# Kernel tuning notes

Hardware: AMD Instinct MI355X
Metric: run time of the kernel (lower is better)

Reference implementation:

```python
import jax, jax.numpy as jnp
import numpy as np

N = 50000      # nodes
E = 800000     # edges (avg degree 16)
DIN = 128
H = 128
DOUT = 64


def setup_inputs() -> dict:
    key = jax.random.key(0)
    ks = jax.random.split(key, 8)
    x = jax.random.normal(ks[0], (N, DIN), dtype=jnp.float32)
    edge_index = jax.random.randint(ks[1], (2, E), 0, N, dtype=jnp.int32)
    def glorot(k, fi, fo):
        return jax.random.normal(k, (fi, fo), dtype=jnp.float32) * (1.0 / np.sqrt(fi))
    return {
        "x": x,
        "edge_index": edge_index,
        "W1": glorot(ks[2], DIN, H), "b1": jnp.zeros((H,), jnp.float32),
        "W2": glorot(ks[3], H, H),   "b2": jnp.zeros((H,), jnp.float32),
        "W3": glorot(ks[4], H, DOUT),"b3": jnp.zeros((DOUT,), jnp.float32),
    }


def reference(x, edge_index, W1, b1, W2, b2, W3, b3):
    n = x.shape[0]
    # GCNConv: add self-loops, symmetric degree normalization D^-1/2 (A+I) D^-1/2
    loop = jnp.arange(n, dtype=edge_index.dtype)
    src = jnp.concatenate([edge_index[0], loop])  # [E+N]
    dst = jnp.concatenate([edge_index[1], loop])
    deg = jax.ops.segment_sum(jnp.ones(src.shape, x.dtype), dst, num_segments=n)
    dinv = jnp.where(deg > 0, jax.lax.rsqrt(deg), 0.0)
    norm = dinv[src] * dinv[dst]  # [E+N]

    def conv(h, W, b):
        h = h @ W                                   # [N, out]
        msg = h[src] * norm[:, None]                # gather + scale
        return jax.ops.segment_sum(msg, dst, num_segments=n) + b

    # gelu after every layer except the last (forward breaks before act)
    h = jax.nn.gelu(conv(x, W1, b1), approximate=False)
    h = jax.nn.gelu(conv(h, W2, b2), approximate=False)
    return conv(h, W3, b3)
```

## Files before the change

### kernel.cpp

```cpp
#include <hip/hip_runtime.h>
#include <math.h>

#define NDIN 128
#define NHID 128
#define NDOUT 64

typedef _Float16 half2_t __attribute__((ext_vector_type(2)));
typedef _Float16 half4_t __attribute__((ext_vector_type(4)));
typedef _Float16 half8_t __attribute__((ext_vector_type(8)));
typedef float    float4v __attribute__((ext_vector_type(4)));

__device__ __forceinline__ float gelu_exact(float x) {
    return 0.5f * x * (1.0f + erff(x * 0.70710678118654752f));
}


__device__ void wtrans_tile(const float* __restrict__ W, _Float16* __restrict__ Wt,
                            int K, int N, int bx, int by) {
    __shared__ float tile[32][33];
    int tx = threadIdx.x & 31, ty = threadIdx.x >> 5;
    for (int i = 0; i < 32; i += 8) {
        int k = by * 32 + ty + i, nn = bx * 32 + tx;
        tile[ty + i][tx] = (k < K && nn < N) ? W[(size_t)k * N + nn] : 0.f;
    }
    __syncthreads();
    for (int i = 0; i < 32; i += 8) {
        int nn = bx * 32 + ty + i, k = by * 32 + tx;
        if (nn < N && k < K) Wt[(size_t)nn * K + k] = (_Float16)tile[tx][ty + i];
    }
}

__global__ __launch_bounds__(256) void prep0_kernel(
    const float* __restrict__ W1, _Float16* __restrict__ W1t,
    const float* __restrict__ W2, _Float16* __restrict__ W2t,
    const float* __restrict__ W3, _Float16* __restrict__ W3t,
    int* __restrict__ count, int* __restrict__ done, int n) {
    int b = blockIdx.x;
    if (b < 16) {
        wtrans_tile(W1, W1t, NDIN, NHID, b & 3, b >> 2);
    } else if (b < 32) {
        wtrans_tile(W2, W2t, NHID, NHID, (b - 16) & 3, (b - 16) >> 2);
    } else if (b < 40) {
        wtrans_tile(W3, W3t, NHID, NDOUT, (b - 32) & 1, (b - 32) >> 1);
    } else {
        int z = b - 40;
        int i = z * 256 + threadIdx.x;
        if (i < n) count[i] = 0;
        if (z == 0 && threadIdx.x < 64) done[threadIdx.x] = 0;
    }
}


__global__ void count_kernel(const int* __restrict__ dst, int* __restrict__ count, int E) {
    int e = blockIdx.x * blockDim.x + threadIdx.x;
    if (e < E) atomicAdd(&count[dst[e]], 1);
}


__global__ __launch_bounds__(256) void reduce_scan_kernel(
    const int* __restrict__ count, int* __restrict__ blocksum, int* __restrict__ blockoff,
    int* __restrict__ rowptr, float* __restrict__ dinv, int* __restrict__ done,
    int nb, int n) {
    __shared__ int s[256];
    __shared__ int flag;
    __shared__ int boff_s;
    int t = threadIdx.x;
    int i = blockIdx.x * 256 + t;
    int v = (i < n) ? count[i] : 0;
    s[t] = v;
    __syncthreads();
    for (int off = 128; off > 0; off >>= 1) {
        if (t < off) s[t] += s[t + off];
        __syncthreads();
    }
    if (t == 0) {
        atomicExch(&blocksum[blockIdx.x], s[0]);
        __threadfence();
        int old = atomicAdd(&done[0], 1);
        flag = (old == nb - 1) ? 1 : 0;
    }
    __syncthreads();
    if (flag) {
        __threadfence();
        int pv = (t < nb) ? atomicAdd(&blocksum[t], 0) : 0;
        s[t] = pv;
        __syncthreads();
        for (int off = 1; off < 256; off <<= 1) {
            int u = (t >= off) ? s[t - off] : 0;
            __syncthreads();
            s[t] += u;
            __syncthreads();
        }
        if (t < nb) atomicExch(&blockoff[t], s[t] - pv);
        if (t == 255) rowptr[n] = s[255];
        __threadfence();
        if (t == 0) atomicExch(&done[1], 1);
    } else if (t == 0) {
        while (atomicAdd(&done[1], 0) == 0) __builtin_amdgcn_s_sleep(2);
        __threadfence();
    }
    __syncthreads();
    if (t == 0) boff_s = atomicAdd(&blockoff[blockIdx.x], 0);
    s[t] = v;
    __syncthreads();
    for (int off = 1; off < 256; off <<= 1) {
        int u = (t >= off) ? s[t - off] : 0;
        __syncthreads();
        s[t] += u;
        __syncthreads();
    }
    if (i < n) {
        rowptr[i] = boff_s + s[t] - v;
        dinv[i] = rsqrtf((float)(v + 1));
    }
}


template <int BN>
__device__ __forceinline__ void gemm_phaseB(
    const _Float16 (*lds_a)[136], const _Float16* __restrict__ Bt,
    _Float16* __restrict__ T, int bm, int M) {
    int tid = threadIdx.x;
    int wave = tid >> 6, lane = tid & 63;
    int m = lane & 15, quad = lane >> 4;
    const int NT = BN / 16;
    float4v acc[NT];
#pragma unroll
    for (int nt = 0; nt < NT; nt++) acc[nt] = (float4v){0.f, 0.f, 0.f, 0.f};
    int arow = (wave << 4) + m;
#pragma unroll
    for (int kc = 0; kc < 128; kc += 32) {
        half8_t a = *(const half8_t*)&lds_a[arow][kc + quad * 8];
#pragma unroll
        for (int nt = 0; nt < NT; nt++) {
            half8_t b = *(const half8_t*)&Bt[(size_t)(nt * 16 + m) * 128 + kc + quad * 8];
            acc[nt] = __builtin_amdgcn_mfma_f32_16x16x32_f16(a, b, acc[nt], 0, 0, 0);
        }
    }
#pragma unroll
    for (int nt = 0; nt < NT; nt++) {
#pragma unroll
        for (int r = 0; r < 4; r++) {
            int grow = bm + (wave << 4) + (quad << 2) + r;
            if (grow < M) T[(size_t)grow * BN + nt * 16 + m] = (_Float16)acc[nt][r];
        }
    }
}


__device__ __forceinline__ half2_t agg_node128(
    const half2_t* __restrict__ t2, const int* __restrict__ rowptr,
    const int2* __restrict__ adj, const float* __restrict__ dinv,
    const float* __restrict__ bias, int node, int lane) {
    float wself = dinv[node];
    wself *= wself;
    half2_t v = t2[(size_t)node * 64 + lane];
    float accx = wself * (float)v[0], accy = wself * (float)v[1];
    int beg = rowptr[node], end = rowptr[node + 1];
    for (int e0 = beg; e0 < end; e0 += 64) {
        int rem = end - e0;
        int j = 0; float w = 0.f;
        if (lane < rem) {
            int2 ed = adj[e0 + lane];
            j = ed.x; w = __int_as_float(ed.y);
        }
        int cnt = rem < 64 ? rem : 64;
        for (int c = 0; c < cnt; c += 16) {
#pragma unroll
            for (int i = 0; i < 16; i++) {
                int jj = __builtin_amdgcn_readlane(j, c + i);
                float ww = __int_as_float(
                    __builtin_amdgcn_readlane(__float_as_int(w), c + i));
                half2_t u = t2[(size_t)jj * 64 + lane];
                accx += ww * (float)u[0];
                accy += ww * (float)u[1];
            }
        }
    }
    float2 b = ((const float2*)bias)[lane];
    accx = gelu_exact(accx + b.x);
    accy = gelu_exact(accy + b.y);
    half2_t o; o[0] = (_Float16)accx; o[1] = (_Float16)accy;
    return o;
}


__global__ __launch_bounds__(256) void fill_gemm1_kernel(
    const int* __restrict__ src, const int* __restrict__ dst,
    const float* __restrict__ dinv, const int* __restrict__ rowptr,
    int* __restrict__ count, int2* __restrict__ adj, int E,
    const float* __restrict__ x, const _Float16* __restrict__ W1t,
    _Float16* __restrict__ T, int M, int fillblocks) {
    __shared__ _Float16 lds_a[64][136];
    int b = blockIdx.x;
    if (b < fillblocks) {
        int e = b * 256 + threadIdx.x;
        if (e >= E) return;
        int s = src[e], d = dst[e];
        int slot = atomicSub(&count[d], 1) - 1;
        int p = rowptr[d] + slot;
        adj[p] = make_int2(s, __float_as_int(dinv[s] * dinv[d]));
        return;
    }
    int bm = (b - fillblocks) * 64;
    int tid = threadIdx.x;
#pragma unroll
    for (int j = 0; j < 8; j++) {
        int c = tid + j * 256;
        int r = c >> 5, col = (c & 31) << 2;
        int grow = bm + r;
        float4 v = make_float4(0.f, 0.f, 0.f, 0.f);
        if (grow < M) v = *(const float4*)(x + (size_t)grow * 128 + col);
        half4_t h;
        h[0] = (_Float16)v.x; h[1] = (_Float16)v.y;
        h[2] = (_Float16)v.z; h[3] = (_Float16)v.w;
        *(half4_t*)&lds_a[r][col] = h;
    }
    __syncthreads();
    gemm_phaseB<128>(lds_a, W1t, T, bm, M);
}


template <int BN>
__global__ __launch_bounds__(256, 4) void agg_gemm_kernel(
    const _Float16* __restrict__ t, const int* __restrict__ rowptr,
    const int2* __restrict__ adj, const float* __restrict__ dinv,
    const float* __restrict__ bias, const _Float16* __restrict__ Bt,
    _Float16* __restrict__ T, int M) {
    __shared__ _Float16 lds_a[64][136];
    int tid = threadIdx.x;
    int wave = tid >> 6, lane = tid & 63;
    int bm = blockIdx.x * 64;
    const half2_t* t2 = (const half2_t*)t;
#pragma unroll 1
    for (int p = 0; p < 16; p++) {
        int r = (wave << 4) + p;
        int node = bm + r;
        half2_t o;
        o[0] = (_Float16)0.f; o[1] = (_Float16)0.f;
        if (node < M) o = agg_node128(t2, rowptr, adj, dinv, bias, node, lane);
        *(half2_t*)&lds_a[r][lane << 1] = o;
    }
    __syncthreads();
    gemm_phaseB<BN>(lds_a, Bt, T, bm, M);
}


template <int F, bool DOGELU, bool OUTF16>
__global__ __launch_bounds__(256) void agg_kernel(
    const _Float16* __restrict__ t, const int* __restrict__ rowptr,
    const int2* __restrict__ adj, const float* __restrict__ dinv,
    const float* __restrict__ bias, void* __restrict__ outp, int n) {
    int node = (int)((blockIdx.x * blockDim.x + threadIdx.x) >> 6);
    int lane = threadIdx.x & 63;
    if (node >= n) return;

    float wself = dinv[node];
    wself *= wself;
    int beg = rowptr[node];
    int end = rowptr[node + 1];

    if (F == 128) {
        const half2_t* t2 = (const half2_t*)t;
        half2_t v = t2[(size_t)node * 64 + lane];
        float accx = wself * (float)v[0], accy = wself * (float)v[1];
        for (int e0 = beg; e0 < end; e0 += 64) {
            int rem = end - e0;
            int j = 0; float w = 0.f;
            if (lane < rem) {
                int2 ed = adj[e0 + lane];
                j = ed.x; w = __int_as_float(ed.y);
            }
            int cnt = rem < 64 ? rem : 64;
            for (int c = 0; c < cnt; c += 16) {
#pragma unroll
                for (int i = 0; i < 16; i++) {
                    int jj = __builtin_amdgcn_readlane(j, c + i);
                    float ww = __int_as_float(
                        __builtin_amdgcn_readlane(__float_as_int(w), c + i));
                    half2_t u = t2[(size_t)jj * 64 + lane];
                    accx += ww * (float)u[0];
                    accy += ww * (float)u[1];
                }
            }
        }
        float2 b = ((const float2*)bias)[lane];
        accx += b.x; accy += b.y;
        if (DOGELU) { accx = gelu_exact(accx); accy = gelu_exact(accy); }
        if (OUTF16) {
            half2_t o; o[0] = (_Float16)accx; o[1] = (_Float16)accy;
            ((half2_t*)outp)[(size_t)node * 64 + lane] = o;
        } else {
            float2 o; o.x = accx; o.y = accy;
            ((float2*)outp)[(size_t)node * 64 + lane] = o;
        }
    } else {
        float acc = wself * (float)t[(size_t)node * 64 + lane];
        for (int e0 = beg; e0 < end; e0 += 64) {
            int rem = end - e0;
            int j = 0; float w = 0.f;
            if (lane < rem) {
                int2 ed = adj[e0 + lane];
                j = ed.x; w = __int_as_float(ed.y);
            }
            int cnt = rem < 64 ? rem : 64;
            for (int c = 0; c < cnt; c += 16) {
#pragma unroll
                for (int i = 0; i < 16; i++) {
                    int jj = __builtin_amdgcn_readlane(j, c + i);
                    float ww = __int_as_float(
                        __builtin_amdgcn_readlane(__float_as_int(w), c + i));
                    acc += ww * (float)t[(size_t)jj * 64 + lane];
                }
            }
        }
        acc += bias[lane];
        if (DOGELU) acc = gelu_exact(acc);
        if (OUTF16) ((_Float16*)outp)[(size_t)node * 64 + lane] = (_Float16)acc;
        else        ((float*)outp)[(size_t)node * 64 + lane] = acc;
    }
}


extern "C" void kernel_launch(void* const* d_in, const int* in_sizes, int n_in,
                              void* d_out, int out_size, void* d_ws, size_t ws_size,
                              hipStream_t stream) {
    const float* x  = (const float*)d_in[0];
    const int* edge = (const int*)d_in[1];
    const float* W1 = (const float*)d_in[2];
    const float* b1 = (const float*)d_in[3];
    const float* W2 = (const float*)d_in[4];
    const float* b2 = (const float*)d_in[5];
    const float* W3 = (const float*)d_in[6];
    const float* b3 = (const float*)d_in[7];
    float* out = (float*)d_out;

    const int N = in_sizes[0] / NDIN;
    const int E = in_sizes[1] / 2;
    const int* src = edge;
    const int* dst = edge + E;
    const int NB = (N + 255) / 256;

    char* p = (char*)d_ws;
    auto alloc = [&](size_t bytes) {
        char* q = p;
        p += (bytes + 255) & ~(size_t)255;
        return q;
    };
    int*       count    = (int*)alloc((size_t)N * 4);
    int*       rowptr   = (int*)alloc((size_t)(N + 1) * 4);
    int*       blocksum = (int*)alloc((size_t)NB * 4);
    int*       blockoff = (int*)alloc((size_t)NB * 4);
    int*       done     = (int*)alloc(256);
    float*     dinv     = (float*)alloc((size_t)N * 4);
    int2*      adj      = (int2*)alloc((size_t)E * 8);
    _Float16*  W1t      = (_Float16*)alloc((size_t)NHID * NDIN * 2);
    _Float16*  W2t      = (_Float16*)alloc((size_t)NHID * NHID * 2);
    _Float16*  W3t      = (_Float16*)alloc((size_t)NDOUT * NHID * 2);
    _Float16*  tbuf     = (_Float16*)alloc((size_t)N * NHID * 2);
    _Float16*  hbuf     = (_Float16*)alloc((size_t)N * NHID * 2);

    dim3 blk(256);
    int mtiles = (N + 63) / 64;
    int eblocks = (E + 255) / 256;
    int agg_blocks = (N + 3) / 4;

    prep0_kernel<<<40 + NB, blk, 0, stream>>>(W1, W1t, W2, W2t, W3, W3t, count, done, N);
    count_kernel<<<eblocks, blk, 0, stream>>>(dst, count, E);
    reduce_scan_kernel<<<NB, blk, 0, stream>>>(count, blocksum, blockoff, rowptr,
                                               dinv, done, NB, N);
    fill_gemm1_kernel<<<eblocks + mtiles, blk, 0, stream>>>(
        src, dst, dinv, rowptr, count, adj, E, x, W1t, tbuf, N, eblocks);
    agg_gemm_kernel<128><<<mtiles, blk, 0, stream>>>(tbuf, rowptr, adj, dinv, b1,
                                                     W2t, hbuf, N);
    agg_gemm_kernel<64><<<mtiles, blk, 0, stream>>>(hbuf, rowptr, adj, dinv, b2,
                                                    W3t, tbuf, N);
    agg_kernel<64, false, false><<<agg_blocks, blk, 0, stream>>>(tbuf, rowptr, adj,
                                                                 dinv, b3, out, N);
}
```

Measured before the change: 324.3 us.

## Split fill and layer-1 GEMM, shrink fused agg-GEMM tiles to 16 rows

The fused fill+GEMM1 launch is split into a standalone fill kernel and a separate MFMA GEMM kernel that stages W1t in LDS. The fused aggregate+GEMM kernels now handle 16 nodes per block instead of 64, with the four waves splitting the output columns. This launches four times as many blocks, which should balance load better across irregular node degrees and reduce per-block serial aggregation. The cost is an extra kernel launch, the loss of overlap between the fill and GEMM1 work, and weights being reread from global/L2 by many more blocks.

```diff
diff --git a/kernel.cpp b/kernel.cpp
--- a/kernel.cpp
+++ b/kernel.cpp
@@ -116,24 +116,77 @@
 }
 
 
-template <int BN>
-__device__ __forceinline__ void gemm_phaseB(
-    const _Float16 (*lds_a)[136], const _Float16* __restrict__ Bt,
-    _Float16* __restrict__ T, int bm, int M) {
+__global__ void fill_kernel(const int* __restrict__ src, const int* __restrict__ dst,
+                            const float* __restrict__ dinv, const int* __restrict__ rowptr,
+                            int* __restrict__ count, int2* __restrict__ adj, int E) {
+    int e = blockIdx.x * blockDim.x + threadIdx.x;
+    if (e >= E) return;
+    int s = src[e], d = dst[e];
+    int slot = atomicSub(&count[d], 1) - 1;
+    int p = rowptr[d] + slot;
+    adj[p] = make_int2(s, __float_as_int(dinv[s] * dinv[d]));
+}
+
+
+template <int BN, bool AF16>
+__global__ __launch_bounds__(256) void gemm_mfma(
+    const void* __restrict__ Aptr, const _Float16* __restrict__ Bt,
+    _Float16* __restrict__ T, int M) {
+    __shared__ _Float16 lds_a[64][136];
+    __shared__ _Float16 lds_bt[BN][136];
+    const int K = 128;
     int tid = threadIdx.x;
+    int bm = blockIdx.x * 64;
     int wave = tid >> 6, lane = tid & 63;
     int m = lane & 15, quad = lane >> 4;
+
+    if (AF16) {
+        const _Float16* A = (const _Float16*)Aptr;
+#pragma unroll
+        for (int j = 0; j < 4; j++) {
+            int c = tid + j * 256;
+            int r = c >> 4, col = (c & 15) << 3;
+            int grow = bm + r;
+            uint4 v = make_uint4(0, 0, 0, 0);
+            if (grow < M) v = *(const uint4*)(A + (size_t)grow * K + col);
+            *(uint4*)&lds_a[r][col] = v;
+        }
+    } else {
+        const float* A = (const float*)Aptr;
+#pragma unroll
+        for (int j = 0; j < 8; j++) {
+            int c = tid + j * 256;
+            int r = c >> 5, col = (c & 31) << 2;
+            int grow = bm + r;
+            float4 v = make_float4(0.f, 0.f, 0.f, 0.f);
+            if (grow < M) v = *(const float4*)(A + (size_t)grow * K + col);
+            half4_t h;
+            h[0] = (_Float16)v.x; h[1] = (_Float16)v.y;
+            h[2] = (_Float16)v.z; h[3] = (_Float16)v.w;
+            *(half4_t*)&lds_a[r][col] = h;
+        }
+    }
+    {
+        const int chunks = BN * K / 8;
+        for (int c = tid; c < chunks; c += 256) {
+            int r = c >> 4, col = (c & 15) << 3;
+            *(uint4*)&lds_bt[r][col] = *(const uint4*)(Bt + (size_t)r * K + col);
+        }
+    }
+    __syncthreads();
+
     const int NT = BN / 16;
     float4v acc[NT];
 #pragma unroll
     for (int nt = 0; nt < NT; nt++) acc[nt] = (float4v){0.f, 0.f, 0.f, 0.f};
+
     int arow = (wave << 4) + m;
 #pragma unroll
-    for (int kc = 0; kc < 128; kc += 32) {
+    for (int kc = 0; kc < K; kc += 32) {
         half8_t a = *(const half8_t*)&lds_a[arow][kc + quad * 8];
 #pragma unroll
         for (int nt = 0; nt < NT; nt++) {
-            half8_t b = *(const half8_t*)&Bt[(size_t)(nt * 16 + m) * 128 + kc + quad * 8];
+            half8_t b = *(const half8_t*)&lds_bt[nt * 16 + m][kc + quad * 8];
             acc[nt] = __builtin_amdgcn_mfma_f32_16x16x32_f16(a, b, acc[nt], 0, 0, 0);
         }
     }
@@ -185,56 +238,20 @@
 }
 
 
-__global__ __launch_bounds__(256) void fill_gemm1_kernel(
-    const int* __restrict__ src, const int* __restrict__ dst,
-    const float* __restrict__ dinv, const int* __restrict__ rowptr,
-    int* __restrict__ count, int2* __restrict__ adj, int E,
-    const float* __restrict__ x, const _Float16* __restrict__ W1t,
-    _Float16* __restrict__ T, int M, int fillblocks) {
-    __shared__ _Float16 lds_a[64][136];
-    int b = blockIdx.x;
-    if (b < fillblocks) {
-        int e = b * 256 + threadIdx.x;
-        if (e >= E) return;
-        int s = src[e], d = dst[e];
-        int slot = atomicSub(&count[d], 1) - 1;
-        int p = rowptr[d] + slot;
-        adj[p] = make_int2(s, __float_as_int(dinv[s] * dinv[d]));
-        return;
-    }
-    int bm = (b - fillblocks) * 64;
-    int tid = threadIdx.x;
-#pragma unroll
-    for (int j = 0; j < 8; j++) {
-        int c = tid + j * 256;
-        int r = c >> 5, col = (c & 31) << 2;
-        int grow = bm + r;
-        float4 v = make_float4(0.f, 0.f, 0.f, 0.f);
-        if (grow < M) v = *(const float4*)(x + (size_t)grow * 128 + col);
-        half4_t h;
-        h[0] = (_Float16)v.x; h[1] = (_Float16)v.y;
-        h[2] = (_Float16)v.z; h[3] = (_Float16)v.w;
-        *(half4_t*)&lds_a[r][col] = h;
-    }
-    __syncthreads();
-    gemm_phaseB<128>(lds_a, W1t, T, bm, M);
-}
-
-
 template <int BN>
-__global__ __launch_bounds__(256, 4) void agg_gemm_kernel(
+__global__ __launch_bounds__(256) void agg_gemm16_kernel(
     const _Float16* __restrict__ t, const int* __restrict__ rowptr,
     const int2* __restrict__ adj, const float* __restrict__ dinv,
     const float* __restrict__ bias, const _Float16* __restrict__ Bt,
     _Float16* __restrict__ T, int M) {
-    __shared__ _Float16 lds_a[64][136];
+    __shared__ _Float16 lds_a[16][136];
     int tid = threadIdx.x;
     int wave = tid >> 6, lane = tid & 63;
-    int bm = blockIdx.x * 64;
+    int bm = blockIdx.x * 16;
     const half2_t* t2 = (const half2_t*)t;
 #pragma unroll 1
-    for (int p = 0; p < 16; p++) {
-        int r = (wave << 4) + p;
+    for (int p = 0; p < 4; p++) {
+        int r = (wave << 2) + p;
         int node = bm + r;
         half2_t o;
         o[0] = (_Float16)0.f; o[1] = (_Float16)0.f;
@@ -242,7 +259,31 @@
         *(half2_t*)&lds_a[r][lane << 1] = o;
     }
     __syncthreads();
-    gemm_phaseB<BN>(lds_a, Bt, T, bm, M);
+
+    int m = lane & 15, quad = lane >> 4;
+    const int NT = BN / 64;
+    float4v acc[NT];
+#pragma unroll
+    for (int nt = 0; nt < NT; nt++) acc[nt] = (float4v){0.f, 0.f, 0.f, 0.f};
+#pragma unroll
+    for (int kc = 0; kc < 128; kc += 32) {
+        half8_t a = *(const half8_t*)&lds_a[m][kc + quad * 8];
+#pragma unroll
+        for (int nt = 0; nt < NT; nt++) {
+            int col = wave * (BN / 4) + nt * 16 + m;
+            half8_t b = *(const half8_t*)&Bt[(size_t)col * 128 + kc + quad * 8];
+            acc[nt] = __builtin_amdgcn_mfma_f32_16x16x32_f16(a, b, acc[nt], 0, 0, 0);
+        }
+    }
+#pragma unroll
+    for (int nt = 0; nt < NT; nt++) {
+#pragma unroll
+        for (int r = 0; r < 4; r++) {
+            int grow = bm + (quad << 2) + r;
+            int col = wave * (BN / 4) + nt * 16 + m;
+            if (grow < M) T[(size_t)grow * BN + col] = (_Float16)acc[nt][r];
+        }
+    }
 }
 
 
@@ -362,6 +403,7 @@
 
     dim3 blk(256);
     int mtiles = (N + 63) / 64;
+    int ntiles16 = (N + 15) / 16;
     int eblocks = (E + 255) / 256;
     int agg_blocks = (N + 3) / 4;
 
@@ -369,12 +411,12 @@
     count_kernel<<<eblocks, blk, 0, stream>>>(dst, count, E);
     reduce_scan_kernel<<<NB, blk, 0, stream>>>(count, blocksum, blockoff, rowptr,
                                                dinv, done, NB, N);
-    fill_gemm1_kernel<<<eblocks + mtiles, blk, 0, stream>>>(
-        src, dst, dinv, rowptr, count, adj, E, x, W1t, tbuf, N, eblocks);
-    agg_gemm_kernel<128><<<mtiles, blk, 0, stream>>>(tbuf, rowptr, adj, dinv, b1,
-                                                     W2t, hbuf, N);
-    agg_gemm_kernel<64><<<mtiles, blk, 0, stream>>>(hbuf, rowptr, adj, dinv, b2,
-                                                    W3t, tbuf, N);
+    fill_kernel<<<eblocks, blk, 0, stream>>>(src, dst, dinv, rowptr, count, adj, E);
+    gemm_mfma<128, false><<<mtiles, blk, 0, stream>>>(x, W1t, tbuf, N);
+    agg_gemm16_kernel<128><<<ntiles16, blk, 0, stream>>>(tbuf, rowptr, adj, dinv, b1,
+                                                         W2t, hbuf, N);
+    agg_gemm16_kernel<64><<<ntiles16, blk, 0, stream>>>(hbuf, rowptr, adj, dinv, b2,
+                                                        W3t, tbuf, N);
     agg_kernel<64, false, false><<<agg_blocks, blk, 0, stream>>>(tbuf, rowptr, adj,
                                                                  dinv, b3, out, N);
 }
```

Measured after the change: 289.5 us. -10.7%, faster.
